# Optimization experiments

Hardware: AMD Instinct MI355X
Metric: run time of the kernel (lower is better)

## Reference

```python
import jax, jax.numpy as jnp
import numpy as np

B, S, D, H = 1, 2048, 768, 12
E, K, I = 8, 2, 1024          # routed experts, top-k, expert inter dim
IS = 2 * I                    # shared-expert inter dim (n_shared_experts * moe_inter_dim)
EPS = 1e-5
ROUTE_SCALE = 1.0


def rmsnorm(x, w, eps=EPS):
    xf = x.astype(jnp.float32)
    return (xf * jax.lax.rsqrt(jnp.mean(xf * xf, axis=-1, keepdims=True) + eps)).astype(x.dtype) * w


def setup_inputs() -> dict:
    key = jax.random.key(0)
    ks = jax.random.split(key, 8)
    sc = 0.02
    return {
        "x": jax.random.normal(ks[0], (B, S, D), jnp.float32),
        "norm1_w": jnp.ones((D,), jnp.float32),
        "norm3_w": jnp.ones((D,), jnp.float32),
        "gate_w": jax.random.normal(ks[1], (E, D), jnp.float32) * sc,
        "w1": jax.random.normal(ks[2], (E, I, D), jnp.float32) * sc,
        "b1": jnp.zeros((E, I), jnp.float32),
        "w2": jax.random.normal(ks[3], (E, D, I), jnp.float32) * sc,
        "b2": jnp.zeros((E, D), jnp.float32),
        "w3": jax.random.normal(ks[4], (E, I, D), jnp.float32) * sc,
        "b3": jnp.zeros((E, I), jnp.float32),
        "fc1_w": jax.random.normal(ks[5], (IS, D), jnp.float32) * sc,
        "fc1_b": jnp.zeros((IS,), jnp.float32),
        "fc2_w": jax.random.normal(ks[6], (D, IS), jnp.float32) * sc,
        "fc2_b": jnp.zeros((D,), jnp.float32),
    }


def _forward(x, norm1_w, norm3_w, gate_w, w1, b1, w2, b2, w3, b3,
             fc1_w, fc1_b, fc2_w, fc2_b):
    b, s, d = x.shape
    hd = d // H

    # ---- self-attention (no qkv/out projections in the original module) ----
    xn = rmsnorm(x, norm1_w)
    qkv = xn.reshape(b, s, H, hd).transpose(0, 2, 1, 3)      # [b,h,s,hd]
    scores = jnp.einsum("bhqd,bhkd->bhqk", qkv, qkv) / np.sqrt(hd)
    attn = jax.nn.softmax(scores, axis=-1)
    ao = jnp.einsum("bhqk,bhkd->bhqd", attn, qkv)
    attn_out = ao.transpose(0, 2, 1, 3).reshape(b, s, d)
    out = x + attn_out

    # ---- MoE on norm3(out) ----
    xf = rmsnorm(out, norm3_w).reshape(-1, d)                # [N, D]
    n = xf.shape[0]

    # Gate: softmax scoring, n_groups=1 (no group masking), no bias (dim != 7168)
    logits = xf @ gate_w.T                                    # [N, E]
    sc = jax.nn.softmax(logits.astype(jnp.float32), axis=-1)  # max-subtract folded in
    _, idx = jax.lax.top_k(sc, K)                             # [N, K]
    weights = jnp.take_along_axis(sc, idx, axis=-1)
    weights = jnp.clip(weights, 1e-7) * ROUTE_SCALE
    weights = weights.astype(xf.dtype)

    # combine matrix: per-token dense expert weights (zeros for unselected)
    cmb = jnp.zeros((n, E), xf.dtype).at[jnp.arange(n)[:, None], idx].add(weights)

    # SwiGLU experts, batched over E (zero combine weight == not dispatched)
    a = jnp.einsum("nd,eid->nei", xf, w1) + b1                # [N,E,I]
    g = jnp.einsum("nd,eid->nei", xf, w3) + b3
    h = jax.nn.silu(a) * g
    eo = jnp.einsum("nei,edi->ned", h, w2) + b2               # [N,E,D]
    y = jnp.einsum("ned,ne->nd", eo, cmb)

    # shared experts (SiLU MLP)
    z = jax.nn.silu(xf @ fc1_w.T + fc1_b) @ fc2_w.T + fc2_b

    moe_out = (y + z).reshape(b, s, d)
    return out + moe_out


def reference(x, norm1_w, norm3_w, gate_w, w1, b1, w2, b2, w3, b3,
              fc1_w, fc1_b, fc2_w, fc2_b):
    return _forward(x, norm1_w, norm3_w, gate_w, w1, b1, w2, b2, w3, b3,
                    fc1_w, fc1_b, fc2_w, fc2_b)
```

## Files before the change

### kernel.cpp

```cpp
#include <hip/hip_runtime.h>
#include <math.h>

#define SEQ    2048
#define DMODEL 768
#define NHEAD  12
#define NEXP   8
#define IDIM   1024
#define ISH    2048
#define KVS    4
#define NE2    10
#define ATTN_BLOCKS 1536
#define CVT_BLOCKS 10752
#define QK_SCALE 0.18033688011112042f

typedef unsigned short u16;
typedef short s16x8 __attribute__((ext_vector_type(8)));
typedef u16   u16x8 __attribute__((ext_vector_type(8)));
typedef float f32x4 __attribute__((ext_vector_type(4)));

#define MFMA_BF16(a, b, c) __builtin_amdgcn_mfma_f32_16x16x32_bf16((a), (b), (c), 0, 0, 0)

__device__ __forceinline__ void glds16(const void* g, void* l) {
  __builtin_amdgcn_global_load_lds(
      (const __attribute__((address_space(1))) unsigned int*)g,
      (__attribute__((address_space(3))) unsigned int*)l, 16, 0, 0);
}

__device__ __forceinline__ u16 f2b(float f) {
  unsigned int u = __float_as_uint(f);
  unsigned int r = u + 0x7fffu + ((u >> 16) & 1u);
  return (u16)(r >> 16);
}
__device__ __forceinline__ float b2f(u16 v) {
  return __uint_as_float(((unsigned int)v) << 16);
}

__global__ __launch_bounds__(256) void rmsnorm_kernel(const float* __restrict__ x,
                                                      const float* __restrict__ n1w,
                                                      u16* __restrict__ xnb,
                                                      int* __restrict__ counts) {
  const int tid = threadIdx.x;
  if (blockIdx.x == 0 && tid < 16) counts[tid] = 0;
  const int lane = tid & 63, w = tid >> 6;
  const int row = blockIdx.x * 4 + w;
  const float* r = x + (size_t)row * DMODEL;
  float v[12];
  float ss = 0.f;
#pragma unroll
  for (int i = 0; i < 12; i++) { v[i] = r[i * 64 + lane]; ss += v[i] * v[i]; }
#pragma unroll
  for (int off = 32; off >= 1; off >>= 1) ss += __shfl_xor(ss, off, 64);
  float rms = rsqrtf(ss * (1.f / DMODEL) + 1e-5f);
  u16* ob = xnb + (size_t)row * DMODEL;
#pragma unroll
  for (int i = 0; i < 12; i++) ob[i * 64 + lane] = f2b(v[i] * rms * n1w[i * 64 + lane]);
}

__global__ __launch_bounds__(256) void attn_cvt_kernel(
    const u16* __restrict__ xnb, u16* __restrict__ Opart,
    float* __restrict__ Mpart, float* __restrict__ Lpart,
    const float* __restrict__ w1, const float* __restrict__ w3, const float* __restrict__ w2,
    const float* __restrict__ fc1, const float* __restrict__ fc2,
    u16* __restrict__ w1b, u16* __restrict__ w3b, u16* __restrict__ w2b,
    u16* __restrict__ fc1b, u16* __restrict__ fc2b) {
  const int tid = threadIdx.x;
  if (blockIdx.x >= ATTN_BLOCKS) {
    long i = (long)(blockIdx.x - ATTN_BLOCKS) * 256 + tid;
    const long NW8 = (long)NEXP * IDIM * DMODEL / 8;
    const long NF8 = (long)ISH * DMODEL / 8;
    const float* s; u16* d; long o;
    if      (i < NW8)             { s = w1;  d = w1b;  o = i; }
    else if (i < 2 * NW8)         { s = w3;  d = w3b;  o = i - NW8; }
    else if (i < 3 * NW8)         { s = w2;  d = w2b;  o = i - 2 * NW8; }
    else if (i < 3 * NW8 + NF8)   { s = fc1; d = fc1b; o = i - 3 * NW8; }
    else                          { s = fc2; d = fc2b; o = i - 3 * NW8 - NF8; }
    float4 a = ((const float4*)s)[2 * o], b = ((const float4*)s)[2 * o + 1];
    u16x8 v;
    v[0] = f2b(a.x); v[1] = f2b(a.y); v[2] = f2b(a.z); v[3] = f2b(a.w);
    v[4] = f2b(b.x); v[5] = f2b(b.y); v[6] = f2b(b.z); v[7] = f2b(b.w);
    ((u16x8*)d)[o] = v;
    return;
  }
  __shared__ u16 QP[64][64];
  __shared__ u16 Ks[64][64];
  __shared__ u16 Vt[64][64];
  const int q0 = (blockIdx.x & 31) * 64;
  const int h = (blockIdx.x >> 5) % NHEAD;
  const int kvs = blockIdx.x / (32 * NHEAD);
  const int lane = tid & 63, w = tid >> 6;
  const int quad = lane >> 4, l15 = lane & 15;
  const size_t hoff = (size_t)h * 64;

  const int lr8 = lane >> 3, b7 = lane & 7;
  const int sch0 = (b7 ^ (lr8 >> 1)) * 8;
  const int sch1 = (b7 ^ (4 + (lr8 >> 1))) * 8;
  const int rkey = (l15 >> 1) & 7;
  const int cb0 = (quad ^ rkey) * 8;
  const int cb1 = ((4 + quad) ^ rkey) * 8;

  glds16(xnb + (size_t)(q0 + 16 * w + lr8) * DMODEL + hoff + sch0, &QP[16 * w][0]);
  glds16(xnb + (size_t)(q0 + 16 * w + 8 + lr8) * DMODEL + hoff + sch1, &QP[16 * w + 8][0]);
  __syncthreads();
  const s16x8 aq0 = *(const s16x8*)&QP[16 * w + l15][cb0];
  const s16x8 aq1 = *(const s16x8*)&QP[16 * w + l15][cb1];

  f32x4 o[4] = {};
  float mrow[4], lrow[4];
#pragma unroll
  for (int r = 0; r < 4; r++) { mrow[r] = -INFINITY; lrow[r] = 0.f; }

  const int it0 = kvs * (SEQ / 64 / KVS);
  for (int it = 0; it < SEQ / 64 / KVS; it++) {
    const int k0 = (it0 + it) * 64;
    glds16(xnb + (size_t)(k0 + 16 * w + lr8) * DMODEL + hoff + sch0, &Ks[16 * w][0]);
    glds16(xnb + (size_t)(k0 + 16 * w + 8 + lr8) * DMODEL + hoff + sch1, &Ks[16 * w + 8][0]);
    __syncthreads();

    {
      const int rp = tid & 31, dcc = (tid >> 5) & 7;
      const int tc = (dcc ^ (rp & 7)) * 8;
      u16x8 v0 = *(const u16x8*)&Ks[2 * rp][tc];
      u16x8 v1 = *(const u16x8*)&Ks[2 * rp + 1][tc];
#pragma unroll
      for (int j = 0; j < 8; j++) {
        const int vrow = dcc * 8 + j;
        const int vkey = (vrow >> 1) & 7;
        *(unsigned int*)&Vt[vrow][((rp >> 2) ^ vkey) * 8 + (rp & 3) * 2] =
            (unsigned int)v0[j] | ((unsigned int)v1[j] << 16);
      }
    }

    f32x4 s4[4] = {};
    __builtin_amdgcn_s_setprio(1);
#pragma unroll
    for (int jt = 0; jt < 4; jt++) {
      s16x8 b0 = *(const s16x8*)&Ks[16 * jt + l15][cb0];
      s16x8 b1 = *(const s16x8*)&Ks[16 * jt + l15][cb1];
      s4[jt] = MFMA_BF16(aq0, b0, s4[jt]);
      s4[jt] = MFMA_BF16(aq1, b1, s4[jt]);
      s4[jt] *= QK_SCALE;
    }
    __builtin_amdgcn_s_setprio(0);

#pragma unroll
    for (int r = 0; r < 4; r++) {
      float mx = mrow[r];
#pragma unroll
      for (int jt = 0; jt < 4; jt++) mx = fmaxf(mx, s4[jt][r]);
#pragma unroll
      for (int m = 1; m <= 8; m <<= 1) mx = fmaxf(mx, __shfl_xor(mx, m, 64));
      float al = exp2f(mrow[r] - mx);
      mrow[r] = mx;
      float pv[4], sum = 0.f;
#pragma unroll
      for (int jt = 0; jt < 4; jt++) { pv[jt] = exp2f(s4[jt][r] - mx); sum += pv[jt]; }
#pragma unroll
      for (int m = 1; m <= 8; m <<= 1) sum += __shfl_xor(sum, m, 64);
      lrow[r] = lrow[r] * al + sum;
#pragma unroll
      for (int jt = 0; jt < 4; jt++) o[jt][r] *= al;
      const int pkey = ((quad * 4 + r) >> 1) & 7;
#pragma unroll
      for (int jt = 0; jt < 4; jt++)
        QP[16 * w + quad * 4 + r][((2 * jt + (l15 >> 3)) ^ pkey) * 8 + (l15 & 7)] =
            f2b(pv[jt]);
    }
    __syncthreads();

    s16x8 ap0 = *(const s16x8*)&QP[16 * w + l15][cb0];
    s16x8 ap1 = *(const s16x8*)&QP[16 * w + l15][cb1];
    __builtin_amdgcn_s_setprio(1);
#pragma unroll
    for (int jt = 0; jt < 4; jt++) {
      s16x8 bv0 = *(const s16x8*)&Vt[16 * jt + l15][cb0];
      s16x8 bv1 = *(const s16x8*)&Vt[16 * jt + l15][cb1];
      o[jt] = MFMA_BF16(ap0, bv0, o[jt]);
      o[jt] = MFMA_BF16(ap1, bv1, o[jt]);
    }
    __builtin_amdgcn_s_setprio(0);
  }

  const int hk = h * KVS + kvs;
#pragma unroll
  for (int r = 0; r < 4; r++) {
    int q = q0 + 16 * w + quad * 4 + r;
    size_t base = (size_t)q * (KVS * NHEAD) + hk;
#pragma unroll
    for (int jt = 0; jt < 4; jt++)
      Opart[base * 64 + 16 * jt + l15] = f2b(o[jt][r]);
    if (l15 == 0) {
      Mpart[base] = mrow[r];
      Lpart[base] = lrow[r];
    }
  }
}

__global__ __launch_bounds__(256) void fused_post_kernel(
    const u16* __restrict__ Opart, const float* __restrict__ Mpart,
    const float* __restrict__ Lpart, const float* __restrict__ x,
    const float* __restrict__ n3w, const float* __restrict__ gw,
    u16* __restrict__ xfb, float* __restrict__ out,
    int* __restrict__ counts, int* __restrict__ toklist, float* __restrict__ wtlist) {
  const int t = blockIdx.x;
  const int tid = threadIdx.x;
  const int lane = tid & 63, w = tid >> 6;
  __shared__ u16 Os[48 * 64];
  __shared__ float MsLs[96];
  __shared__ float ssP[4];
  __shared__ float geP[4][NEXP];

  const u16* orow = Opart + (size_t)t * (48 * 64);
  for (int c = tid; c < 384; c += 256)
    *(u16x8*)&Os[c * 8] = *(const u16x8*)&orow[c * 8];
  if (tid < 96)
    MsLs[tid] = (tid < 48) ? Mpart[(size_t)t * 48 + tid]
                           : Lpart[(size_t)t * 48 + (tid - 48)];
  __syncthreads();

  float val[3];
  float ss = 0.f;
  const float* xr = x + (size_t)t * DMODEL;
  float* outr = out + (size_t)t * DMODEL;
#pragma unroll
  for (int j = 0; j < 3; j++) {
    const int ii = 3 * w + j;
    float m0 = MsLs[ii * 4 + 0], m1 = MsLs[ii * 4 + 1];
    float m2 = MsLs[ii * 4 + 2], m3 = MsLs[ii * 4 + 3];
    float mh = fmaxf(fmaxf(m0, m1), fmaxf(m2, m3));
    float c0 = exp2f(m0 - mh), c1 = exp2f(m1 - mh);
    float c2 = exp2f(m2 - mh), c3 = exp2f(m3 - mh);
    float Lh = c0 * MsLs[48 + ii * 4 + 0] + c1 * MsLs[48 + ii * 4 + 1] +
               c2 * MsLs[48 + ii * 4 + 2] + c3 * MsLs[48 + ii * 4 + 3];
    float O = c0 * b2f(Os[(ii * 4 + 0) * 64 + lane]) +
              c1 * b2f(Os[(ii * 4 + 1) * 64 + lane]) +
              c2 * b2f(Os[(ii * 4 + 2) * 64 + lane]) +
              c3 * b2f(Os[(ii * 4 + 3) * 64 + lane]);
    float v = xr[ii * 64 + lane] + O / Lh;
    outr[ii * 64 + lane] = v;
    val[j] = v;
    ss += v * v;
  }
#pragma unroll
  for (int off = 32; off >= 1; off >>= 1) ss += __shfl_xor(ss, off, 64);
  if (lane == 0) ssP[w] = ss;
  __syncthreads();
  float rms = rsqrtf((ssP[0] + ssP[1] + ssP[2] + ssP[3]) * (1.f / DMODEL) + 1e-5f);

  float ge[NEXP] = {};
#pragma unroll
  for (int j = 0; j < 3; j++) {
    int c = (3 * w + j) * 64 + lane;
    float xn = val[j] * rms * n3w[c];
    xfb[(size_t)t * DMODEL + c] = f2b(xn);
#pragma unroll
    for (int e = 0; e < NEXP; e++) ge[e] = fmaf(xn, gw[e * DMODEL + c], ge[e]);
  }
#pragma unroll
  for (int off = 32; off >= 1; off >>= 1)
#pragma unroll
    for (int e = 0; e < NEXP; e++) ge[e] += __shfl_xor(ge[e], off, 64);
  if (lane == 0)
#pragma unroll
    for (int e = 0; e < NEXP; e++) geP[w][e] = ge[e];
  __syncthreads();

  if (tid == 0) {
    float p[NEXP], mx = -INFINITY, s = 0.f;
#pragma unroll
    for (int e = 0; e < NEXP; e++) {
      p[e] = geP[0][e] + geP[1][e] + geP[2][e] + geP[3][e];
      mx = fmaxf(mx, p[e]);
    }
#pragma unroll
    for (int e = 0; e < NEXP; e++) { p[e] = __expf(p[e] - mx); s += p[e]; }
    int e0 = 0; float b0 = p[0];
    for (int e = 1; e < NEXP; e++) if (p[e] > b0) { b0 = p[e]; e0 = e; }
    int e1 = -1; float b1v = -1.f;
    for (int e = 0; e < NEXP; e++) if (e != e0 && p[e] > b1v) { b1v = p[e]; e1 = e; }
    float inv = 1.f / s;
    int pos0 = atomicAdd(&counts[e0], 1);
    toklist[e0 * SEQ + pos0] = t;
    wtlist[e0 * SEQ + pos0] = fmaxf(b0 * inv, 1e-7f);
    int pos1 = atomicAdd(&counts[e1], 1);
    toklist[e1 * SEQ + pos1] = t;
    wtlist[e1 * SEQ + pos1] = fmaxf(b1v * inv, 1e-7f);
  }
}

__global__ __launch_bounds__(256) void gemm1_kernel(
    const u16* __restrict__ xfb,
    const u16* __restrict__ w1b, const u16* __restrict__ w3b, const u16* __restrict__ fc1b,
    const float* __restrict__ b1, const float* __restrict__ b3, const float* __restrict__ fc1_b,
    const int* __restrict__ counts, const int* __restrict__ toklist, u16* __restrict__ hb) {
  __shared__ u16 As[64][64];
  __shared__ u16 W1s[64][64];
  __shared__ u16 W3s[64][64];
  __shared__ int rIdx[64];
  const int e = blockIdx.z;
  const bool routed = (e < NEXP);
  int cnt, off;
  if (routed) {
    cnt = counts[e];
    off = 0;
    for (int i = 0; i < e; i++) off += counts[i];
  } else {
    cnt = SEQ;
    off = 2 * SEQ + (e - NEXP) * SEQ;
  }
  const int m0 = blockIdx.y * 64;
  if (m0 >= cnt) return;
  const int n0 = blockIdx.x * 64;
  const int tid = threadIdx.x;
  if (tid < 64) {
    int rr = m0 + tid;
    rIdx[tid] = routed ? toklist[e * SEQ + (rr < cnt ? rr : cnt - 1)] : rr;
  }
  __syncthreads();
  const u16* W1 = routed ? w1b + (size_t)e * IDIM * DMODEL
                         : fc1b + (size_t)(e - NEXP) * IDIM * DMODEL;
  const ptrdiff_t d31 = w3b - w1b;

  const int lane = tid & 63, w = tid >> 6;
  const int quad = lane >> 4, l15 = lane & 15;
  const int wy = w >> 1, wx = w & 1;
  const int lr8 = lane >> 3;
  const int sch = ((lane & 7) ^ lr8) * 8;

  const u16 *aS[2], *w1S[2];
#pragma unroll
  for (int c = 0; c < 2; c++) {
    int tr = 16 * w + 8 * c + lr8;
    aS[c]  = xfb + (size_t)rIdx[tr] * DMODEL + sch;
    w1S[c] = W1 + (size_t)(n0 + tr) * DMODEL + sch;
  }

  f32x4 acc1[2][2] = {};
  f32x4 acc3[2][2] = {};
  for (int k0 = 0; k0 < DMODEL; k0 += 64) {
#pragma unroll
    for (int c = 0; c < 2; c++) glds16(aS[c] + k0, &As[16 * w + 8 * c][0]);
#pragma unroll
    for (int c = 0; c < 2; c++) glds16(w1S[c] + k0, &W1s[16 * w + 8 * c][0]);
    if (routed) {
#pragma unroll
      for (int c = 0; c < 2; c++) glds16(w1S[c] + d31 + k0, &W3s[16 * w + 8 * c][0]);
    }
    __syncthreads();
#pragma unroll
    for (int kk = 0; kk < 2; kk++) {
      const int cb = (((kk * 4 + quad) ^ (l15 & 7))) * 8;
      s16x8 af[2], w1f[2];
#pragma unroll
      for (int i = 0; i < 2; i++) af[i] = *(const s16x8*)&As[32 * wy + 16 * i + l15][cb];
#pragma unroll
      for (int j = 0; j < 2; j++) w1f[j] = *(const s16x8*)&W1s[32 * wx + 16 * j + l15][cb];
#pragma unroll
      for (int i = 0; i < 2; i++)
#pragma unroll
        for (int j = 0; j < 2; j++)
          acc1[i][j] = MFMA_BF16(af[i], w1f[j], acc1[i][j]);
      if (routed) {
        s16x8 w3f[2];
#pragma unroll
        for (int j = 0; j < 2; j++) w3f[j] = *(const s16x8*)&W3s[32 * wx + 16 * j + l15][cb];
#pragma unroll
        for (int i = 0; i < 2; i++)
#pragma unroll
          for (int j = 0; j < 2; j++)
            acc3[i][j] = MFMA_BF16(af[i], w3f[j], acc3[i][j]);
      }
    }
    __syncthreads();
  }

#pragma unroll
  for (int j = 0; j < 2; j++) {
    int n = n0 + 32 * wx + 16 * j + l15;
    float b1v = routed ? b1[e * IDIM + n] : fc1_b[(e - NEXP) * IDIM + n];
    float b3v = routed ? b3[e * IDIM + n] : 0.f;
#pragma unroll
    for (int i = 0; i < 2; i++) {
#pragma unroll
      for (int r = 0; r < 4; r++) {
        int rr = m0 + 32 * wy + 16 * i + quad * 4 + r;
        if (rr < cnt) {
          float a = acc1[i][j][r] + b1v;
          float g = routed ? (acc3[i][j][r] + b3v) : 1.f;
          float hv = a / (1.f + __expf(-a)) * g;
          hb[(size_t)(off + rr) * IDIM + n] = f2b(hv);
        }
      }
    }
  }
}

__global__ __launch_bounds__(256) void gemm2_kernel(
    const u16* __restrict__ hb,
    const u16* __restrict__ w2b, const u16* __restrict__ fc2b,
    const float* __restrict__ b2, const float* __restrict__ fc2_b,
    const int* __restrict__ counts, const int* __restrict__ toklist,
    const float* __restrict__ wtlist, float* __restrict__ out) {
  __shared__ u16 As[64][64];
  __shared__ u16 Ws[64][64];
  const int n0 = blockIdx.x * 64;
  if (n0 >= DMODEL) return;
  const int e = blockIdx.z;
  const bool routed = (e < NEXP);
  int cnt, off;
  if (routed) {
    cnt = counts[e];
    off = 0;
    for (int i = 0; i < e; i++) off += counts[i];
  } else {
    cnt = SEQ;
    off = 2 * SEQ + (e - NEXP) * SEQ;
  }
  const int m0 = blockIdx.y * 64;
  if (m0 >= cnt) return;
  const int tid = threadIdx.x;

  const u16* Wb; int ldw, kof;
  if (routed) { Wb = w2b + (size_t)e * DMODEL * IDIM; ldw = IDIM; kof = 0; }
  else        { Wb = fc2b;                            ldw = ISH;  kof = (e - NEXP) * IDIM; }

  const int lane = tid & 63, w = tid >> 6;
  const int quad = lane >> 4, l15 = lane & 15;
  const int wy = w >> 1, wx = w & 1;
  const int lr8 = lane >> 3;
  const int sch = ((lane & 7) ^ lr8) * 8;

  const u16 *aS[2], *wS[2];
#pragma unroll
  for (int c = 0; c < 2; c++) {
    int tr = 16 * w + 8 * c + lr8;
    int ra = m0 + tr;
    ra = off + (ra < cnt ? ra : cnt - 1);
    aS[c] = hb + (size_t)ra * IDIM + sch;
    wS[c] = Wb + (size_t)(n0 + tr) * ldw + kof + sch;
  }

  f32x4 acc[2][2] = {};
  for (int k0 = 0; k0 < IDIM; k0 += 64) {
#pragma unroll
    for (int c = 0; c < 2; c++) glds16(aS[c] + k0, &As[16 * w + 8 * c][0]);
#pragma unroll
    for (int c = 0; c < 2; c++) glds16(wS[c] + k0, &Ws[16 * w + 8 * c][0]);
    __syncthreads();
#pragma unroll
    for (int kk = 0; kk < 2; kk++) {
      const int cb = (((kk * 4 + quad) ^ (l15 & 7))) * 8;
      s16x8 af[2], wf[2];
#pragma unroll
      for (int i = 0; i < 2; i++) af[i] = *(const s16x8*)&As[32 * wy + 16 * i + l15][cb];
#pragma unroll
      for (int j = 0; j < 2; j++) wf[j] = *(const s16x8*)&Ws[32 * wx + 16 * j + l15][cb];
#pragma unroll
      for (int i = 0; i < 2; i++)
#pragma unroll
        for (int j = 0; j < 2; j++)
          acc[i][j] = MFMA_BF16(af[i], wf[j], acc[i][j]);
    }
    __syncthreads();
  }

#pragma unroll
  for (int j = 0; j < 2; j++) {
    int n = n0 + 32 * wx + 16 * j + l15;
    float bv = routed ? b2[e * DMODEL + n] : (e == NEXP ? fc2_b[n] : 0.f);
#pragma unroll
    for (int i = 0; i < 2; i++) {
#pragma unroll
      for (int r = 0; r < 4; r++) {
        int rr = m0 + 32 * wy + 16 * i + quad * 4 + r;
        if (rr < cnt) {
          int tok; float wt;
          if (routed) { tok = toklist[e * SEQ + rr]; wt = wtlist[e * SEQ + rr]; }
          else        { tok = rr;                    wt = 1.f; }
          atomicAdd(&out[(size_t)tok * DMODEL + n], wt * (acc[i][j][r] + bv));
        }
      }
    }
  }
}

extern "C" void kernel_launch(void* const* d_in, const int* in_sizes, int n_in,
                              void* d_out, int out_size, void* d_ws, size_t ws_size,
                              hipStream_t stream) {
  const float* x       = (const float*)d_in[0];
  const float* norm1_w = (const float*)d_in[1];
  const float* norm3_w = (const float*)d_in[2];
  const float* gate_w  = (const float*)d_in[3];
  const float* w1      = (const float*)d_in[4];
  const float* b1      = (const float*)d_in[5];
  const float* w2      = (const float*)d_in[6];
  const float* b2      = (const float*)d_in[7];
  const float* w3      = (const float*)d_in[8];
  const float* b3      = (const float*)d_in[9];
  const float* fc1_w   = (const float*)d_in[10];
  const float* fc1_b   = (const float*)d_in[11];
  const float* fc2_w   = (const float*)d_in[12];
  const float* fc2_b   = (const float*)d_in[13];
  float* out = (float*)d_out;

  char* p = (char*)d_ws;
  u16*   xnb    = (u16*)p;   p += (size_t)SEQ * DMODEL * 2;
  u16*   xfb    = (u16*)p;   p += (size_t)SEQ * DMODEL * 2;
  u16*   hb     = (u16*)p;   p += (size_t)4 * SEQ * IDIM * 2;
  u16*   Opart  = (u16*)p;   p += (size_t)KVS * NHEAD * SEQ * 64 * 2;
  float* Mpart  = (float*)p; p += (size_t)KVS * NHEAD * SEQ * 4;
  float* Lpart  = (float*)p; p += (size_t)KVS * NHEAD * SEQ * 4;
  u16*   w1b    = (u16*)p;   p += (size_t)NEXP * IDIM * DMODEL * 2;
  u16*   w3b    = (u16*)p;   p += (size_t)NEXP * IDIM * DMODEL * 2;
  u16*   w2b    = (u16*)p;   p += (size_t)NEXP * DMODEL * IDIM * 2;
  u16*   fc1b   = (u16*)p;   p += (size_t)ISH * DMODEL * 2;
  u16*   fc2b   = (u16*)p;   p += (size_t)DMODEL * ISH * 2;
  int*   counts = (int*)p;   p += 256;
  int*   toklist= (int*)p;   p += (size_t)NEXP * SEQ * 4;
  float* wtlist = (float*)p; p += (size_t)NEXP * SEQ * 4;

  rmsnorm_kernel<<<SEQ / 4, 256, 0, stream>>>(x, norm1_w, xnb, counts);
  attn_cvt_kernel<<<ATTN_BLOCKS + CVT_BLOCKS, 256, 0, stream>>>(
      xnb, Opart, Mpart, Lpart, w1, w3, w2, fc1_w, fc2_w,
      w1b, w3b, w2b, fc1b, fc2b);
  fused_post_kernel<<<SEQ, 256, 0, stream>>>(Opart, Mpart, Lpart, x, norm3_w, gate_w,
                                             xfb, out, counts, toklist, wtlist);
  gemm1_kernel<<<dim3(IDIM / 64, SEQ / 64, NE2), 256, 0, stream>>>(
      xfb, w1b, w3b, fc1b, b1, b3, fc1_b, counts, toklist, hb);
  gemm2_kernel<<<dim3(16, SEQ / 64, NE2), 256, 0, stream>>>(
      hb, w2b, fc2b, b2, fc2_b, counts, toklist, wtlist, out);
  (void)in_sizes; (void)n_in; (void)out_size; (void)ws_size;
}
```

Before: 313.5 us.

## Double-buffer attention K tiles and move w2/fc2 conversion into gemm1 launch

The attention loop now double-buffers K tiles in shared memory and prefetches the next tile while the current one is processed, hiding global-to-LDS latency. The fp32-to-bf16 weight conversion is split. w1/w3/fc1 are still converted alongside attention, with two 8-element chunks per thread, while w2/fc2 conversion moves into extra z-slices of the gemm1 launch so it overlaps routed GEMM work. This trades more LDS per attention block and a larger gemm1 grid for a shorter critical path through the attention kernel.

```diff
diff --git a/kernel.cpp b/kernel.cpp
--- a/kernel.cpp
+++ b/kernel.cpp
@@ -10,7 +10,7 @@
 #define KVS    4
 #define NE2    10
 #define ATTN_BLOCKS 1536
-#define CVT_BLOCKS 10752
+#define CVT1_BLOCKS 3456
 #define QK_SCALE 0.18033688011112042f
 
 typedef unsigned short u16;
@@ -33,6 +33,14 @@
 }
 __device__ __forceinline__ float b2f(u16 v) {
   return __uint_as_float(((unsigned int)v) << 16);
+}
+
+__device__ __forceinline__ void cvt8(const float* s, u16* d, long o) {
+  float4 a = ((const float4*)s)[2 * o], b = ((const float4*)s)[2 * o + 1];
+  u16x8 v;
+  v[0] = f2b(a.x); v[1] = f2b(a.y); v[2] = f2b(a.z); v[3] = f2b(a.w);
+  v[4] = f2b(b.x); v[5] = f2b(b.y); v[6] = f2b(b.z); v[7] = f2b(b.w);
+  ((u16x8*)d)[o] = v;
 }
 
 __global__ __launch_bounds__(256) void rmsnorm_kernel(const float* __restrict__ x,
@@ -59,30 +67,22 @@
 __global__ __launch_bounds__(256) void attn_cvt_kernel(
     const u16* __restrict__ xnb, u16* __restrict__ Opart,
     float* __restrict__ Mpart, float* __restrict__ Lpart,
-    const float* __restrict__ w1, const float* __restrict__ w3, const float* __restrict__ w2,
-    const float* __restrict__ fc1, const float* __restrict__ fc2,
-    u16* __restrict__ w1b, u16* __restrict__ w3b, u16* __restrict__ w2b,
-    u16* __restrict__ fc1b, u16* __restrict__ fc2b) {
+    const float* __restrict__ w1, const float* __restrict__ w3, const float* __restrict__ fc1,
+    u16* __restrict__ w1b, u16* __restrict__ w3b, u16* __restrict__ fc1b) {
   const int tid = threadIdx.x;
   if (blockIdx.x >= ATTN_BLOCKS) {
-    long i = (long)(blockIdx.x - ATTN_BLOCKS) * 256 + tid;
+    long i0 = (long)(blockIdx.x - ATTN_BLOCKS) * 512 + tid * 2;
     const long NW8 = (long)NEXP * IDIM * DMODEL / 8;
-    const long NF8 = (long)ISH * DMODEL / 8;
     const float* s; u16* d; long o;
-    if      (i < NW8)             { s = w1;  d = w1b;  o = i; }
-    else if (i < 2 * NW8)         { s = w3;  d = w3b;  o = i - NW8; }
-    else if (i < 3 * NW8)         { s = w2;  d = w2b;  o = i - 2 * NW8; }
-    else if (i < 3 * NW8 + NF8)   { s = fc1; d = fc1b; o = i - 3 * NW8; }
-    else                          { s = fc2; d = fc2b; o = i - 3 * NW8 - NF8; }
-    float4 a = ((const float4*)s)[2 * o], b = ((const float4*)s)[2 * o + 1];
-    u16x8 v;
-    v[0] = f2b(a.x); v[1] = f2b(a.y); v[2] = f2b(a.z); v[3] = f2b(a.w);
-    v[4] = f2b(b.x); v[5] = f2b(b.y); v[6] = f2b(b.z); v[7] = f2b(b.w);
-    ((u16x8*)d)[o] = v;
+    if      (i0 < NW8)      { s = w1;  d = w1b;  o = i0; }
+    else if (i0 < 2 * NW8)  { s = w3;  d = w3b;  o = i0 - NW8; }
+    else                    { s = fc1; d = fc1b; o = i0 - 2 * NW8; }
+    cvt8(s, d, o);
+    cvt8(s, d, o + 1);
     return;
   }
   __shared__ u16 QP[64][64];
-  __shared__ u16 Ks[64][64];
+  __shared__ u16 Ks[2][64][64];
   __shared__ u16 Vt[64][64];
   const int q0 = (blockIdx.x & 31) * 64;
   const int h = (blockIdx.x >> 5) % NHEAD;
@@ -98,8 +98,16 @@
   const int cb0 = (quad ^ rkey) * 8;
   const int cb1 = ((4 + quad) ^ rkey) * 8;
 
+  const int it0 = kvs * (SEQ / 64 / KVS);
+  const int NIT = SEQ / 64 / KVS;
+
   glds16(xnb + (size_t)(q0 + 16 * w + lr8) * DMODEL + hoff + sch0, &QP[16 * w][0]);
   glds16(xnb + (size_t)(q0 + 16 * w + 8 + lr8) * DMODEL + hoff + sch1, &QP[16 * w + 8][0]);
+  {
+    const int k0 = it0 * 64;
+    glds16(xnb + (size_t)(k0 + 16 * w + lr8) * DMODEL + hoff + sch0, &Ks[0][16 * w][0]);
+    glds16(xnb + (size_t)(k0 + 16 * w + 8 + lr8) * DMODEL + hoff + sch1, &Ks[0][16 * w + 8][0]);
+  }
   __syncthreads();
   const s16x8 aq0 = *(const s16x8*)&QP[16 * w + l15][cb0];
   const s16x8 aq1 = *(const s16x8*)&QP[16 * w + l15][cb1];
@@ -109,18 +117,23 @@
 #pragma unroll
   for (int r = 0; r < 4; r++) { mrow[r] = -INFINITY; lrow[r] = 0.f; }
 
-  const int it0 = kvs * (SEQ / 64 / KVS);
-  for (int it = 0; it < SEQ / 64 / KVS; it++) {
-    const int k0 = (it0 + it) * 64;
-    glds16(xnb + (size_t)(k0 + 16 * w + lr8) * DMODEL + hoff + sch0, &Ks[16 * w][0]);
-    glds16(xnb + (size_t)(k0 + 16 * w + 8 + lr8) * DMODEL + hoff + sch1, &Ks[16 * w + 8][0]);
+  int cur = 0;
+  for (int it = 0; it < NIT; it++) {
     __syncthreads();
+
+    if (it + 1 < NIT) {
+      const int kn = (it0 + it + 1) * 64;
+      glds16(xnb + (size_t)(kn + 16 * w + lr8) * DMODEL + hoff + sch0,
+             &Ks[cur ^ 1][16 * w][0]);
+      glds16(xnb + (size_t)(kn + 16 * w + 8 + lr8) * DMODEL + hoff + sch1,
+             &Ks[cur ^ 1][16 * w + 8][0]);
+    }
 
     {
       const int rp = tid & 31, dcc = (tid >> 5) & 7;
       const int tc = (dcc ^ (rp & 7)) * 8;
-      u16x8 v0 = *(const u16x8*)&Ks[2 * rp][tc];
-      u16x8 v1 = *(const u16x8*)&Ks[2 * rp + 1][tc];
+      u16x8 v0 = *(const u16x8*)&Ks[cur][2 * rp][tc];
+      u16x8 v1 = *(const u16x8*)&Ks[cur][2 * rp + 1][tc];
 #pragma unroll
       for (int j = 0; j < 8; j++) {
         const int vrow = dcc * 8 + j;
@@ -134,8 +147,8 @@
     __builtin_amdgcn_s_setprio(1);
 #pragma unroll
     for (int jt = 0; jt < 4; jt++) {
-      s16x8 b0 = *(const s16x8*)&Ks[16 * jt + l15][cb0];
-      s16x8 b1 = *(const s16x8*)&Ks[16 * jt + l15][cb1];
+      s16x8 b0 = *(const s16x8*)&Ks[cur][16 * jt + l15][cb0];
+      s16x8 b1 = *(const s16x8*)&Ks[cur][16 * jt + l15][cb1];
       s4[jt] = MFMA_BF16(aq0, b0, s4[jt]);
       s4[jt] = MFMA_BF16(aq1, b1, s4[jt]);
       s4[jt] *= QK_SCALE;
@@ -178,6 +191,7 @@
       o[jt] = MFMA_BF16(ap1, bv1, o[jt]);
     }
     __builtin_amdgcn_s_setprio(0);
+    cur ^= 1;
   }
 
   const int hk = h * KVS + kvs;
@@ -291,7 +305,19 @@
     const u16* __restrict__ xfb,
     const u16* __restrict__ w1b, const u16* __restrict__ w3b, const u16* __restrict__ fc1b,
     const float* __restrict__ b1, const float* __restrict__ b3, const float* __restrict__ fc1_b,
-    const int* __restrict__ counts, const int* __restrict__ toklist, u16* __restrict__ hb) {
+    const int* __restrict__ counts, const int* __restrict__ toklist, u16* __restrict__ hb,
+    const float* __restrict__ w2f, const float* __restrict__ fc2f,
+    u16* __restrict__ w2b, u16* __restrict__ fc2b) {
+  const int tid = threadIdx.x;
+  if (blockIdx.z >= NE2) {
+    long i = ((long)(blockIdx.z - NE2) * 512 + blockIdx.y * 16 + blockIdx.x) * 256 + tid;
+    const long NW8 = (long)NEXP * IDIM * DMODEL / 8;
+    const long NF8 = (long)ISH * DMODEL / 8;
+    if (i >= NW8 + NF8) return;
+    if (i < NW8) cvt8(w2f, w2b, i);
+    else         cvt8(fc2f, fc2b, i - NW8);
+    return;
+  }
   __shared__ u16 As[64][64];
   __shared__ u16 W1s[64][64];
   __shared__ u16 W3s[64][64];
@@ -310,7 +336,6 @@
   const int m0 = blockIdx.y * 64;
   if (m0 >= cnt) return;
   const int n0 = blockIdx.x * 64;
-  const int tid = threadIdx.x;
   if (tid < 64) {
     int rr = m0 + tid;
     rIdx[tid] = routed ? toklist[e * SEQ + (rr < cnt ? rr : cnt - 1)] : rr;
@@ -519,13 +544,13 @@
   float* wtlist = (float*)p; p += (size_t)NEXP * SEQ * 4;
 
   rmsnorm_kernel<<<SEQ / 4, 256, 0, stream>>>(x, norm1_w, xnb, counts);
-  attn_cvt_kernel<<<ATTN_BLOCKS + CVT_BLOCKS, 256, 0, stream>>>(
-      xnb, Opart, Mpart, Lpart, w1, w3, w2, fc1_w, fc2_w,
-      w1b, w3b, w2b, fc1b, fc2b);
+  attn_cvt_kernel<<<ATTN_BLOCKS + CVT1_BLOCKS, 256, 0, stream>>>(
+      xnb, Opart, Mpart, Lpart, w1, w3, fc1_w, w1b, w3b, fc1b);
   fused_post_kernel<<<SEQ, 256, 0, stream>>>(Opart, Mpart, Lpart, x, norm3_w, gate_w,
                                              xfb, out, counts, toklist, wtlist);
-  gemm1_kernel<<<dim3(IDIM / 64, SEQ / 64, NE2), 256, 0, stream>>>(
-      xfb, w1b, w3b, fc1b, b1, b3, fc1_b, counts, toklist, hb);
+  gemm1_kernel<<<dim3(IDIM / 64, SEQ / 64, NE2 + 8), 256, 0, stream>>>(
+      xfb, w1b, w3b, fc1b, b1, b3, fc1_b, counts, toklist, hb,
+      w2, fc2_w, w2b, fc2b);
   gemm2_kernel<<<dim3(16, SEQ / 64, NE2), 256, 0, stream>>>(
       hb, w2b, fc2b, b2, fc2_b, counts, toklist, wtlist, out);
   (void)in_sizes; (void)n_in; (void)out_size; (void)ws_size;
```

Result: no change. 311.0 us (-0.8%).
